# Kernel tuning notes

Hardware: AMD Instinct MI355X
Metric: run time of the kernel (lower is better)

Reference implementation:

```python
import jax, jax.numpy as jnp
import numpy as np

B, S, D, H = 2, 4096, 512, 8
HD = D // H  # head_dim = 64


def setup_inputs() -> dict:
    key = jax.random.key(0)
    ks = jax.random.split(key, 12)
    scale = 0.02
    inp = {
        "q": jax.random.normal(ks[0], (B, S, D), dtype=jnp.float32),
        "k": jax.random.normal(ks[1], (B, S, D), dtype=jnp.float32),
        "v": jax.random.normal(ks[2], (B, S, D), dtype=jnp.float32),
        "mask": jax.random.randint(ks[3], (B, S, S), 0, 2, dtype=jnp.int32),
        "wq_kernel": jax.random.normal(ks[4], (D, D), dtype=jnp.float32) * scale,
        "wq_bias": jnp.zeros((D,), dtype=jnp.float32),
        "wk_kernel": jax.random.normal(ks[5], (D, D), dtype=jnp.float32) * scale,
        "wk_bias": jnp.zeros((D,), dtype=jnp.float32),
        "wv_kernel": jax.random.normal(ks[6], (D, D), dtype=jnp.float32) * scale,
        "wv_bias": jnp.zeros((D,), dtype=jnp.float32),
        "wo_kernel": jax.random.normal(ks[7], (D, D), dtype=jnp.float32) * scale,
        "wo_bias": jnp.zeros((D,), dtype=jnp.float32),
    }
    return inp


def reference(q, k, v, mask, wq_kernel, wq_bias, wk_kernel, wk_bias,
              wv_kernel, wv_bias, wo_kernel, wo_bias):
    # Dense projections
    qp = q @ wq_kernel + wq_bias            # [B,S,D]
    kp = k @ wk_kernel + wk_bias
    vp = v @ wv_kernel + wv_bias

    def split_heads(x):
        # [B,S,D] -> [B,H,S,HD]
        return x.reshape(B, S, H, HD).transpose(0, 2, 1, 3)

    qh, kh, vh = split_heads(qp), split_heads(kp), split_heads(vp)

    # Scaled dot-product attention (materializes full [B,H,S,S] scores,
    # faithful to the original unfused implementation's math)
    scores = jnp.einsum('bhqd,bhkd->bhqk', qh, kh) / jnp.sqrt(
        jnp.asarray(HD, dtype=jnp.float32))
    scores = scores + mask.astype(jnp.float32)[:, None, :, :] * (-1e9)
    attn = jax.nn.softmax(scores, axis=-1)
    out = jnp.einsum('bhqk,bhkd->bhqd', attn, vh)   # [B,H,S,HD]

    # merge heads: [B,H,S,HD] -> [B,S,D]
    out = out.transpose(0, 2, 1, 3).reshape(B, S, D)
    return out @ wo_kernel + wo_bias
```

## Files before the change

kernel.cpp:

```cpp
#include <hip/hip_runtime.h>
#include <stdint.h>

#define B_ 2
#define S_ 4096
#define D_ 512
#define H_ 8
#define HD_ 64
#define M_ (B_*S_)

typedef __attribute__((ext_vector_type(8))) short bf16x8;
typedef __attribute__((ext_vector_type(4))) float f32x4;

#define QSCALE (0.125f * 1.44269504088896341f)

__device__ __forceinline__ unsigned short f2bf(float f) {
  union { float f; unsigned u; } un; un.f = f;
  unsigned u = un.u;
  return (unsigned short)((u + 0x7fffu + ((u >> 16) & 1u)) >> 16);
}

__device__ __forceinline__ unsigned cvtpk(float lo, float hi) {
  unsigned r;
  asm("v_cvt_pk_bf16_f32 %0, %1, %2" : "=v"(r) : "v"(lo), "v"(hi));
  return r;
}

__device__ __forceinline__ void gl16(const void* g, void* l) {
  __builtin_amdgcn_global_load_lds(
      (const __attribute__((address_space(1))) void*)g,
      (__attribute__((address_space(3))) void*)l, 16, 0, 0);
}

__device__ __forceinline__ int kperm_inv(int p) {
  return ((p & 0x1C) << 1) | ((p & 0x20) >> 3) | (p & 3);
}

__global__ __launch_bounds__(256) void mpack(const int* __restrict__ mask,
                                             unsigned long long* __restrict__ bits) {
  const int nw = (gridDim.x * 256) >> 6;
  int w = (blockIdx.x * 256 + threadIdx.x) >> 6;
  int lane = threadIdx.x & 63;
  const int NWORD = (int)((size_t)B_ * S_ * S_ / 64);
  for (int word = w; word < NWORD; word += nw) {
    int m = mask[(size_t)word * 64 + lane];
    unsigned long long bal = __ballot(m != 0);
    if (lane == 0) bits[word] = bal;
  }
}

__global__ __launch_bounds__(256) void wtrans4(const float* __restrict__ w0, const float* __restrict__ w1,
                                               const float* __restrict__ w2, const float* __restrict__ w3,
                                               unsigned short* __restrict__ t0, unsigned short* __restrict__ t1,
                                               unsigned short* __restrict__ t2, unsigned short* __restrict__ t3) {
  const float* W = blockIdx.z==0?w0: blockIdx.z==1?w1: blockIdx.z==2?w2:w3;
  unsigned short* T = blockIdx.z==0?t0: blockIdx.z==1?t1: blockIdx.z==2?t2:t3;
  __shared__ float tile[32][33];
  int n0 = blockIdx.x*32, k0 = blockIdx.y*32;
  int tx = threadIdx.x & 31, ty = threadIdx.x >> 5;
  #pragma unroll
  for (int i=0;i<4;i++)
    tile[ty + i*8][tx] = W[(size_t)(k0 + ty + i*8)*D_ + n0 + tx];
  __syncthreads();
  #pragma unroll
  for (int i=0;i<4;i++)
    T[(size_t)(n0 + ty + i*8)*D_ + k0 + tx] = f2bf(tile[tx][ty + i*8]);
}

template<int OUT_MODE, int CONVA>
__device__ __forceinline__ void gemm_body(const void* __restrict__ Ap,
                                          const unsigned short* __restrict__ Wt,
                                          const float* __restrict__ bias,
                                          void* __restrict__ Out, float oscale) {
  __shared__ __align__(16) unsigned short lAB[2*128*64];
  unsigned short* lA = lAB;
  unsigned short* lB = lAB + 128*64;
  int bm = blockIdx.x, bn = blockIdx.y;
  int tid = threadIdx.x, lane = tid & 63, wid = tid >> 6;
  int g = lane >> 4, cc = lane & 15;
  int wm = wid >> 1, wn = wid & 1;

  f32x4 acc[4][4];
  #pragma unroll
  for (int mi=0;mi<4;mi++)
    #pragma unroll
    for (int ni=0;ni<4;ni++)
      acc[mi][ni] = (f32x4){0.f,0.f,0.f,0.f};

  for (int ks = 0; ks < D_; ks += 64) {
    __syncthreads();
    #pragma unroll
    for (int c4 = 0; c4 < 4; c4++) {
      int idx = wid*256 + c4*64 + lane;
      int row = idx >> 3, ch = idx & 7;
      int sw = ch ^ (row & 7);
      bf16x8 va;
      if (CONVA) {
        const float* a32 = (const float*)Ap + (size_t)(bm*128 + row)*D_ + ks + ch*8;
        float4 f0 = *(const float4*)a32;
        float4 f1 = *(const float4*)(a32 + 4);
        union { unsigned d[4]; bf16x8 v; } u;
        u.d[0] = cvtpk(f0.x, f0.y);
        u.d[1] = cvtpk(f0.z, f0.w);
        u.d[2] = cvtpk(f1.x, f1.y);
        u.d[3] = cvtpk(f1.z, f1.w);
        va = u.v;
      } else {
        va = *(const bf16x8*)((const unsigned short*)Ap + (size_t)(bm*128 + row)*D_ + ks + ch*8);
      }
      bf16x8 vb = *(const bf16x8*)(Wt + (size_t)(bn*128 + row)*D_ + ks + ch*8);
      *(bf16x8*)((char*)lA + row*128 + sw*16) = va;
      *(bf16x8*)((char*)lB + row*128 + sw*16) = vb;
    }
    __syncthreads();
    #pragma unroll
    for (int kk = 0; kk < 2; kk++) {
      bf16x8 af[4], bfv[4];
      #pragma unroll
      for (int mi=0;mi<4;mi++) {
        int row = wm*64 + mi*16 + cc;
        af[mi] = *(const bf16x8*)((const char*)lA + row*128 + (((4*kk+g) ^ (row&7))<<4));
      }
      #pragma unroll
      for (int ni=0;ni<4;ni++) {
        int row = wn*64 + ni*16 + cc;
        bfv[ni] = *(const bf16x8*)((const char*)lB + row*128 + (((4*kk+g) ^ (row&7))<<4));
      }
      #pragma unroll
      for (int mi=0;mi<4;mi++)
        #pragma unroll
        for (int ni=0;ni<4;ni++)
          acc[mi][ni] = __builtin_amdgcn_mfma_f32_16x16x32_bf16(af[mi], bfv[ni], acc[mi][ni], 0, 0, 0);
    }
  }

  if (OUT_MODE == 2) {
    __syncthreads();
    char* ldsT = (char*)lAB + wid*8192;
    #pragma unroll
    for (int ni=0;ni<4;ni++) {
      int n_l = ni*16 + cc;
      float bv = bias[bn*128 + wn*64 + n_l];
      #pragma unroll
      for (int mi=0;mi<4;mi++) {
        ushort4 pk;
        pk.x = f2bf(acc[mi][ni][0] + bv);
        pk.y = f2bf(acc[mi][ni][1] + bv);
        pk.z = f2bf(acc[mi][ni][2] + bv);
        pk.w = f2bf(acc[mi][ni][3] + bv);
        *(ushort4*)(ldsT + n_l*128 + ((32*mi + 8*g) ^ ((n_l&7)<<4))) = pk;
      }
    }
    asm volatile("s_waitcnt lgkmcnt(0)" ::: "memory");
    __builtin_amdgcn_sched_barrier(0);
    #pragma unroll
    for (int it=0; it<8; ++it) {
      int task = it*64 + lane;
      int row = task >> 3, ch = task & 7;
      bf16x8 vv = *(const bf16x8*)(ldsT + row*128 + ((ch ^ (row&7))<<4));
      int n_g = bn*128 + wn*64 + row;
      int m_g = bm*128 + wm*64 + ch*8;
      int bb = m_g >> 12, ss = m_g & (S_-1);
      int hh = n_g >> 6, hd = n_g & 63;
      *(bf16x8*)((unsigned short*)Out + (((size_t)(bb*H_+hh)*HD_ + hd)*S_ + ss)) = vv;
    }
    return;
  }

  #pragma unroll
  for (int ni=0;ni<4;ni++) {
    int n = bn*128 + wn*64 + ni*16 + cc;
    float bv = bias[n];
    #pragma unroll
    for (int mi=0;mi<4;mi++) {
      f32x4 vacc = acc[mi][ni];
      #pragma unroll
      for (int j=0;j<4;j++) {
        int r = bm*128 + wm*64 + mi*16 + 4*g + j;
        float val = (vacc[j] + bv) * oscale;
        if (OUT_MODE == 0) {
          int b = r >> 12, s = r & (S_-1);
          int h = n >> 6, hd = n & 63;
          ((unsigned short*)Out)[(((size_t)(b*H_ + h)*S_ + s) << 6) + hd] = f2bf(val);
        } else {
          ((float*)Out)[(size_t)r*D_ + n] = val;
        }
      }
    }
  }
}

__global__ __launch_bounds__(256,3) void qkv_gemm(
    const float* __restrict__ q32, const float* __restrict__ k32, const float* __restrict__ v32,
    const unsigned short* __restrict__ wqt, const unsigned short* __restrict__ wkt,
    const unsigned short* __restrict__ wvt,
    const float* __restrict__ bq, const float* __restrict__ bk, const float* __restrict__ bv,
    unsigned short* __restrict__ Qp, unsigned short* __restrict__ Kp,
    unsigned short* __restrict__ Vt) {
  if (blockIdx.z == 0)      gemm_body<0,1>(q32, wqt, bq, Qp, QSCALE);
  else if (blockIdx.z == 1) gemm_body<0,1>(k32, wkt, bk, Kp, 1.0f);
  else                      gemm_body<2,1>(v32, wvt, bv, Vt, 1.0f);
}

__global__ __launch_bounds__(256,3) void o_gemm(const unsigned short* __restrict__ att,
                                                const unsigned short* __restrict__ wot,
                                                const float* __restrict__ bo,
                                                float* __restrict__ out) {
  gemm_body<1,0>(att, wot, bo, out, 1.0f);
}


#define FA_ISSUE(NCUR, MN0, MN1)                                        \
    { char* kb = lds + (NCUR)*8192 + woff;                              \
      gl16(gkA, kb); gl16(gkB, kb + 4096);                              \
      gl16(gvA, kb + 16384); gl16(gvB, kb + 16384 + 4096);              \
      gkA += 64*HD_; gkB += 64*HD_; gvA += 64; gvB += 64;               \
      MN0 = *mb0p++; MN1 = *mb1p++; }

#define FA_TILE(CUR, MC0, MC1, DOISSUE, MN0, MN1)                             \
  { asm volatile("s_waitcnt vmcnt(0)" ::: "memory");                          \
    __builtin_amdgcn_s_barrier();                                             \
    if (DOISSUE) FA_ISSUE((CUR)^1, MN0, MN1)                                  \
    f32x4 st0[4], st1[4];                                                     \
    __builtin_amdgcn_s_setprio(1);                                            \
    _Pragma("unroll")                                                         \
    for (int t4=0;t4<4;t4++) {                                                \
      bf16x8 ak0 = *(const bf16x8*)(lds + (CUR)*8192 + rdO[t4][0]);           \
      bf16x8 ak1 = *(const bf16x8*)(lds + (CUR)*8192 + rdO[t4][1]);           \
      f32x4 s0 = (f32x4){0.f,0.f,0.f,0.f};                                    \
      s0 = __builtin_amdgcn_mfma_f32_16x16x32_bf16(ak0, aq00, s0, 0,0,0);     \
      s0 = __builtin_amdgcn_mfma_f32_16x16x32_bf16(ak1, aq01, s0, 0,0,0);     \
      f32x4 s1 = (f32x4){0.f,0.f,0.f,0.f};                                    \
      s1 = __builtin_amdgcn_mfma_f32_16x16x32_bf16(ak0, aq10, s1, 0,0,0);     \
      s1 = __builtin_amdgcn_mfma_f32_16x16x32_bf16(ak1, aq11, s1, 0,0,0);     \
      st0[t4] = s0; st1[t4] = s1;                                             \
    }                                                                         \
    __builtin_amdgcn_s_setprio(0);                                            \
    unsigned long long sh0 = MC0 >> g8, sh1 = MC1 >> g8;                      \
    unsigned lo0 = (unsigned)sh0, hi0 = (unsigned)(sh0 >> 32);                \
    unsigned lo1 = (unsigned)sh1, hi1 = (unsigned)(sh1 >> 32);                \
    union { unsigned d[2][4]; bf16x8 v[2]; } P0, P1;                          \
    _Pragma("unroll")                                                         \
    for (int t4=0;t4<4;t4++) {                                                \
      unsigned bm0 = (t4 & 1) ? hi0 : lo0;                                    \
      unsigned bm1 = (t4 & 1) ? hi1 : lo1;                                    \
      const int bb = (t4 >> 1) * 4;                                           \
      float a0 = __builtin_amdgcn_exp2f(st0[t4][0] - mj);                     \
      float a1 = __builtin_amdgcn_exp2f(st0[t4][1] - mj);                     \
      float a2 = __builtin_amdgcn_exp2f(st0[t4][2] - mj);                     \
      float a3 = __builtin_amdgcn_exp2f(st0[t4][3] - mj);                     \
      a0 = (bm0 & (1u<<(bb+0))) ? 0.f : a0;                                   \
      a1 = (bm0 & (1u<<(bb+1))) ? 0.f : a1;                                   \
      a2 = (bm0 & (1u<<(bb+2))) ? 0.f : a2;                                   \
      a3 = (bm0 & (1u<<(bb+3))) ? 0.f : a3;                                   \
      P0.d[t4&1][(t4>>1)*2]   = cvtpk(a0, a1);                                \
      P0.d[t4&1][(t4>>1)*2+1] = cvtpk(a2, a3);                                \
      float c0 = __builtin_amdgcn_exp2f(st1[t4][0] - mj);                     \
      float c1 = __builtin_amdgcn_exp2f(st1[t4][1] - mj);                     \
      float c2 = __builtin_amdgcn_exp2f(st1[t4][2] - mj);                     \
      float c3 = __builtin_amdgcn_exp2f(st1[t4][3] - mj);                     \
      c0 = (bm1 & (1u<<(bb+0))) ? 0.f : c0;                                   \
      c1 = (bm1 & (1u<<(bb+1))) ? 0.f : c1;                                   \
      c2 = (bm1 & (1u<<(bb+2))) ? 0.f : c2;                                   \
      c3 = (bm1 & (1u<<(bb+3))) ? 0.f : c3;                                   \
      P1.d[t4&1][(t4>>1)*2]   = cvtpk(c0, c1);                                \
      P1.d[t4&1][(t4>>1)*2+1] = cvtpk(c2, c3);                                \
    }                                                                         \
    __builtin_amdgcn_s_setprio(1);                                            \
    _Pragma("unroll")                                                         \
    for (int kk=0;kk<2;kk++) {                                                \
      lj40 = __builtin_amdgcn_mfma_f32_16x16x32_bf16(P0.v[kk], vones, lj40, 0,0,0); \
      lj41 = __builtin_amdgcn_mfma_f32_16x16x32_bf16(P1.v[kk], vones, lj41, 0,0,0); \
      _Pragma("unroll")                                                       \
      for (int t4=0;t4<4;t4++) {                                              \
        bf16x8 bv8 = *(const bf16x8*)(lds + 16384 + (CUR)*8192 + rdO[t4][kk]); \
        o20[t4] = __builtin_amdgcn_mfma_f32_16x16x32_bf16(P0.v[kk], bv8, o20[t4], 0,0,0); \
        o21[t4] = __builtin_amdgcn_mfma_f32_16x16x32_bf16(P1.v[kk], bv8, o21[t4], 0,0,0); \
      }                                                                       \
    }                                                                         \
    __builtin_amdgcn_s_setprio(0);                                            \
    float pm0 = fmaxf(fmaxf(fmaxf(st0[0][0],st0[0][1]),fmaxf(st0[0][2],st0[0][3])),  \
                fmaxf(fmaxf(fmaxf(st0[1][0],st0[1][1]),fmaxf(st0[1][2],st0[1][3])),  \
                fmaxf(fmaxf(fmaxf(st0[2][0],st0[2][1]),fmaxf(st0[2][2],st0[2][3])),  \
                      fmaxf(fmaxf(st0[3][0],st0[3][1]),fmaxf(st0[3][2],st0[3][3]))))); \
    float pm1 = fmaxf(fmaxf(fmaxf(st1[0][0],st1[0][1]),fmaxf(st1[0][2],st1[0][3])),  \
                fmaxf(fmaxf(fmaxf(st1[1][0],st1[1][1]),fmaxf(st1[1][2],st1[1][3])),  \
                fmaxf(fmaxf(fmaxf(st1[2][0],st1[2][1]),fmaxf(st1[2][2],st1[2][3])),  \
                      fmaxf(fmaxf(st1[3][0],st1[3][1]),fmaxf(st1[3][2],st1[3][3]))))); \
    float pm = fmaxf(pm0, pm1);                                               \
    if (__any(pm > mj + 7.f)) {                                               \
      pm = fmaxf(pm, __shfl_xor(pm, 16));                                     \
      pm = fmaxf(pm, __shfl_xor(pm, 32));                                     \
      float mn = fmaxf(mj, pm);                                               \
      float alpha = __builtin_amdgcn_exp2f(mj - mn);                          \
      mj = mn;                                                                \
      _Pragma("unroll")                                                       \
      for (int j=0;j<4;j++) {                                                 \
        float aj = __shfl(alpha, 4*g + j);                                    \
        lj40[j] *= aj; lj41[j] *= aj;                                         \
        _Pragma("unroll")                                                     \
        for (int t4=0;t4<4;t4++) { o20[t4][j] *= aj; o21[t4][j] *= aj; }      \
      }                                                                       \
    } }

__global__ __launch_bounds__(256,2) void fattn(const unsigned short* __restrict__ Qp,
                                               const unsigned short* __restrict__ Kp,
                                               const unsigned short* __restrict__ Vt,
                                               const unsigned long long* __restrict__ bits,
                                               unsigned short* __restrict__ attO) {
  __shared__ __align__(16) char lds[32768];
  const int tid = threadIdx.x, lane = tid & 63, wid = tid >> 6;
  const int g = lane >> 4, cc = lane & 15;
  const int g8 = g << 3;

  const int n = blockIdx.x;
  const int xcd = n & 7, idx = n >> 3;
  const int bh = xcd*2 + (idx >> 5);
  const int qb = idx & 31;
  const int b = bh >> 3;
  const int q0w = qb*128 + wid*32;

  const unsigned short* Qb = Qp + (size_t)bh*S_*HD_;
  const unsigned short* Kb = Kp + (size_t)bh*S_*HD_;
  const unsigned short* Vb = Vt + (size_t)bh*HD_*S_;

  bf16x8 aq00 = *(const bf16x8*)(Qb + (size_t)(q0w+cc)*HD_ + g8);
  bf16x8 aq01 = *(const bf16x8*)(Qb + (size_t)(q0w+cc)*HD_ + 32 + g8);
  bf16x8 aq10 = *(const bf16x8*)(Qb + (size_t)(q0w+16+cc)*HD_ + g8);
  bf16x8 aq11 = *(const bf16x8*)(Qb + (size_t)(q0w+16+cc)*HD_ + 32 + g8);

  int rdO[4][2];
  #pragma unroll
  for (int t4=0;t4<4;t4++) {
    int row = t4*16 + cc;
    int base = row*128 + ((g ^ (row&7)) << 4);
    rdO[t4][0] = base;
    rdO[t4][1] = base ^ 64;
  }

  const int p0 = wid*8 + (lane >> 3);
  const int sl = lane & 7;
  const int cK = sl ^ (p0 & 7);
  const unsigned short* gkA = Kb + (size_t)kperm_inv(p0)      *HD_ + cK*8;
  const unsigned short* gkB = Kb + (size_t)kperm_inv(p0 + 32) *HD_ + cK*8;
  const unsigned short* gvA = Vb + (size_t)p0*S_ + cK*8;
  const unsigned short* gvB = gvA + (size_t)32*S_;
  const int woff = wid*1024;

  const unsigned long long* mb0p = bits + ((size_t)(b*S_ + q0w +      cc)) * (S_/64);
  const unsigned long long* mb1p = bits + ((size_t)(b*S_ + q0w + 16 + cc)) * (S_/64);

  union { unsigned d[4]; bf16x8 v; } onesu;
  onesu.d[0] = onesu.d[1] = onesu.d[2] = onesu.d[3] = 0x3F803F80u;
  const bf16x8 vones = onesu.v;

  f32x4 o20[4], o21[4];
  #pragma unroll
  for (int t4=0;t4<4;t4++) { o20[t4] = (f32x4){0.f,0.f,0.f,0.f}; o21[t4] = (f32x4){0.f,0.f,0.f,0.f}; }
  f32x4 lj40 = (f32x4){0.f,0.f,0.f,0.f};
  f32x4 lj41 = (f32x4){0.f,0.f,0.f,0.f};
  float mj = 0.f;

  unsigned long long mA0=0, mA1=0, mB0=0, mB1=0;

  const int NT = S_/64;

  FA_ISSUE(0, mA0, mA1)

  #pragma unroll 1
  for (int t2 = 0; t2 < NT; t2 += 2) {
    FA_TILE(0, mA0, mA1, true,         mB0, mB1)
    FA_TILE(1, mB0, mB1, (t2+2 < NT),  mA0, mA1)
  }

  const int h = bh & (H_-1);
  #pragma unroll
  for (int j=0;j<4;j++) {
    float i0 = __builtin_amdgcn_rcpf(lj40[j]);
    float i1 = __builtin_amdgcn_rcpf(lj41[j]);
    int qr0 = q0w + 4*g + j;
    int qr1 = q0w + 16 + 4*g + j;
    unsigned short* orow0 = attO + ((size_t)b*S_ + qr0)*D_ + h*HD_;
    unsigned short* orow1 = attO + ((size_t)b*S_ + qr1)*D_ + h*HD_;
    #pragma unroll
    for (int t4=0;t4<4;t4++) {
      orow0[t4*16 + cc] = f2bf(o20[t4][j] * i0);
      orow1[t4*16 + cc] = f2bf(o21[t4][j] * i1);
    }
  }
}

extern "C" void kernel_launch(void* const* d_in, const int* in_sizes, int n_in,
                              void* d_out, int out_size, void* d_ws, size_t ws_size,
                              hipStream_t stream) {
  const float* q    = (const float*)d_in[0];
  const float* k    = (const float*)d_in[1];
  const float* v    = (const float*)d_in[2];
  const int*   mask = (const int*)  d_in[3];
  const float* wq   = (const float*)d_in[4];
  const float* bq   = (const float*)d_in[5];
  const float* wk   = (const float*)d_in[6];
  const float* bk   = (const float*)d_in[7];
  const float* wv   = (const float*)d_in[8];
  const float* bv   = (const float*)d_in[9];
  const float* wo   = (const float*)d_in[10];
  const float* bo   = (const float*)d_in[11];

  char* ws = (char*)d_ws;
  const size_t SZ_MAT = (size_t)M_ * D_ * 2;
  const size_t SZ_W   = (size_t)D_ * D_ * 2;
  unsigned short* wqt = (unsigned short*)(ws);
  unsigned short* wkt = (unsigned short*)(ws + SZ_W);
  unsigned short* wvt = (unsigned short*)(ws + 2*SZ_W);
  unsigned short* wot = (unsigned short*)(ws + 3*SZ_W);
  unsigned short* Qp  = (unsigned short*)(ws + 4*SZ_W);
  unsigned short* Kp  = (unsigned short*)(ws + 4*SZ_W + SZ_MAT);
  unsigned short* Vt  = (unsigned short*)(ws + 4*SZ_W + 2*SZ_MAT);
  unsigned short* att = (unsigned short*)(ws + 4*SZ_W + 3*SZ_MAT);
  unsigned long long* bits = (unsigned long long*)(ws + 4*SZ_W + 4*SZ_MAT);

  mpack<<<2048, 256, 0, stream>>>(mask, bits);
  wtrans4<<<dim3(16,16,4), 256, 0, stream>>>(wq, wk, wv, wo, wqt, wkt, wvt, wot);
  qkv_gemm<<<dim3(64,4,3), 256, 0, stream>>>(q, k, v, wqt, wkt, wvt,
                                             bq, bk, bv, Qp, Kp, Vt);
  fattn<<<512, 256, 0, stream>>>(Qp, Kp, Vt, bits, att);
  o_gemm<<<dim3(64,4), 256, 0, stream>>>(att, wot, bo, (float*)d_out);
}
```

Measured before the change: 202.6 us.

## Software-pipeline flash attention with 4-slot K/V ring and QK/softmax overlap

Restructures the attention loop into a 4-stage ring buffer in LDS, doubled to 64KB, with loads issued two tiles ahead and waits relaxed to vmcnt(6). The QK^T of tile t+1 is interleaved with the softmax and PV of tile t, so MFMA work can overlap the exp and masking work and global-load latency. The cost is more LDS per block, which may lower occupancy below the two blocks per CU in launch bounds, and more registers for two score buffers. Out-of-range prefetches are clamped to the last tile, so some redundant loads are issued at the tail.

```diff
diff --git a/kernel.cpp b/kernel.cpp
--- a/kernel.cpp
+++ b/kernel.cpp
@@ -12,6 +12,7 @@
 typedef __attribute__((ext_vector_type(4))) float f32x4;
 
 #define QSCALE (0.125f * 1.44269504088896341f)
+#define MFMA16(A,B,C) __builtin_amdgcn_mfma_f32_16x16x32_bf16((A),(B),(C),0,0,0)
 
 __device__ __forceinline__ unsigned short f2bf(float f) {
   union { float f; unsigned u; } un; un.f = f;
@@ -129,7 +130,7 @@
       for (int mi=0;mi<4;mi++)
         #pragma unroll
         for (int ni=0;ni<4;ni++)
-          acc[mi][ni] = __builtin_amdgcn_mfma_f32_16x16x32_bf16(af[mi], bfv[ni], acc[mi][ni], 0, 0, 0);
+          acc[mi][ni] = MFMA16(af[mi], bfv[ni], acc[mi][ni]);
     }
   }
 
@@ -209,97 +210,97 @@
 }
 
 
-#define FA_ISSUE(NCUR, MN0, MN1)                                        \
-    { char* kb = lds + (NCUR)*8192 + woff;                              \
-      gl16(gkA, kb); gl16(gkB, kb + 4096);                              \
-      gl16(gvA, kb + 16384); gl16(gvB, kb + 16384 + 4096);              \
-      gkA += 64*HD_; gkB += 64*HD_; gvA += 64; gvB += 64;               \
-      MN0 = *mb0p++; MN1 = *mb1p++; }
-
-#define FA_TILE(CUR, MC0, MC1, DOISSUE, MN0, MN1)                             \
-  { asm volatile("s_waitcnt vmcnt(0)" ::: "memory");                          \
-    __builtin_amdgcn_s_barrier();                                             \
-    if (DOISSUE) FA_ISSUE((CUR)^1, MN0, MN1)                                  \
-    f32x4 st0[4], st1[4];                                                     \
-    __builtin_amdgcn_s_setprio(1);                                            \
-    _Pragma("unroll")                                                         \
-    for (int t4=0;t4<4;t4++) {                                                \
-      bf16x8 ak0 = *(const bf16x8*)(lds + (CUR)*8192 + rdO[t4][0]);           \
-      bf16x8 ak1 = *(const bf16x8*)(lds + (CUR)*8192 + rdO[t4][1]);           \
-      f32x4 s0 = (f32x4){0.f,0.f,0.f,0.f};                                    \
-      s0 = __builtin_amdgcn_mfma_f32_16x16x32_bf16(ak0, aq00, s0, 0,0,0);     \
-      s0 = __builtin_amdgcn_mfma_f32_16x16x32_bf16(ak1, aq01, s0, 0,0,0);     \
-      f32x4 s1 = (f32x4){0.f,0.f,0.f,0.f};                                    \
-      s1 = __builtin_amdgcn_mfma_f32_16x16x32_bf16(ak0, aq10, s1, 0,0,0);     \
-      s1 = __builtin_amdgcn_mfma_f32_16x16x32_bf16(ak1, aq11, s1, 0,0,0);     \
-      st0[t4] = s0; st1[t4] = s1;                                             \
-    }                                                                         \
-    __builtin_amdgcn_s_setprio(0);                                            \
-    unsigned long long sh0 = MC0 >> g8, sh1 = MC1 >> g8;                      \
-    unsigned lo0 = (unsigned)sh0, hi0 = (unsigned)(sh0 >> 32);                \
-    unsigned lo1 = (unsigned)sh1, hi1 = (unsigned)(sh1 >> 32);                \
-    union { unsigned d[2][4]; bf16x8 v[2]; } P0, P1;                          \
-    _Pragma("unroll")                                                         \
-    for (int t4=0;t4<4;t4++) {                                                \
-      unsigned bm0 = (t4 & 1) ? hi0 : lo0;                                    \
-      unsigned bm1 = (t4 & 1) ? hi1 : lo1;                                    \
-      const int bb = (t4 >> 1) * 4;                                           \
-      float a0 = __builtin_amdgcn_exp2f(st0[t4][0] - mj);                     \
-      float a1 = __builtin_amdgcn_exp2f(st0[t4][1] - mj);                     \
-      float a2 = __builtin_amdgcn_exp2f(st0[t4][2] - mj);                     \
-      float a3 = __builtin_amdgcn_exp2f(st0[t4][3] - mj);                     \
-      a0 = (bm0 & (1u<<(bb+0))) ? 0.f : a0;                                   \
-      a1 = (bm0 & (1u<<(bb+1))) ? 0.f : a1;                                   \
-      a2 = (bm0 & (1u<<(bb+2))) ? 0.f : a2;                                   \
-      a3 = (bm0 & (1u<<(bb+3))) ? 0.f : a3;                                   \
-      P0.d[t4&1][(t4>>1)*2]   = cvtpk(a0, a1);                                \
-      P0.d[t4&1][(t4>>1)*2+1] = cvtpk(a2, a3);                                \
-      float c0 = __builtin_amdgcn_exp2f(st1[t4][0] - mj);                     \
-      float c1 = __builtin_amdgcn_exp2f(st1[t4][1] - mj);                     \
-      float c2 = __builtin_amdgcn_exp2f(st1[t4][2] - mj);                     \
-      float c3 = __builtin_amdgcn_exp2f(st1[t4][3] - mj);                     \
-      c0 = (bm1 & (1u<<(bb+0))) ? 0.f : c0;                                   \
-      c1 = (bm1 & (1u<<(bb+1))) ? 0.f : c1;                                   \
-      c2 = (bm1 & (1u<<(bb+2))) ? 0.f : c2;                                   \
-      c3 = (bm1 & (1u<<(bb+3))) ? 0.f : c3;                                   \
-      P1.d[t4&1][(t4>>1)*2]   = cvtpk(c0, c1);                                \
-      P1.d[t4&1][(t4>>1)*2+1] = cvtpk(c2, c3);                                \
-    }                                                                         \
-    __builtin_amdgcn_s_setprio(1);                                            \
-    _Pragma("unroll")                                                         \
-    for (int kk=0;kk<2;kk++) {                                                \
-      lj40 = __builtin_amdgcn_mfma_f32_16x16x32_bf16(P0.v[kk], vones, lj40, 0,0,0); \
-      lj41 = __builtin_amdgcn_mfma_f32_16x16x32_bf16(P1.v[kk], vones, lj41, 0,0,0); \
-      _Pragma("unroll")                                                       \
-      for (int t4=0;t4<4;t4++) {                                              \
-        bf16x8 bv8 = *(const bf16x8*)(lds + 16384 + (CUR)*8192 + rdO[t4][kk]); \
-        o20[t4] = __builtin_amdgcn_mfma_f32_16x16x32_bf16(P0.v[kk], bv8, o20[t4], 0,0,0); \
-        o21[t4] = __builtin_amdgcn_mfma_f32_16x16x32_bf16(P1.v[kk], bv8, o21[t4], 0,0,0); \
-      }                                                                       \
-    }                                                                         \
-    __builtin_amdgcn_s_setprio(0);                                            \
-    float pm0 = fmaxf(fmaxf(fmaxf(st0[0][0],st0[0][1]),fmaxf(st0[0][2],st0[0][3])),  \
-                fmaxf(fmaxf(fmaxf(st0[1][0],st0[1][1]),fmaxf(st0[1][2],st0[1][3])),  \
-                fmaxf(fmaxf(fmaxf(st0[2][0],st0[2][1]),fmaxf(st0[2][2],st0[2][3])),  \
-                      fmaxf(fmaxf(st0[3][0],st0[3][1]),fmaxf(st0[3][2],st0[3][3]))))); \
-    float pm1 = fmaxf(fmaxf(fmaxf(st1[0][0],st1[0][1]),fmaxf(st1[0][2],st1[0][3])),  \
-                fmaxf(fmaxf(fmaxf(st1[1][0],st1[1][1]),fmaxf(st1[1][2],st1[1][3])),  \
-                fmaxf(fmaxf(fmaxf(st1[2][0],st1[2][1]),fmaxf(st1[2][2],st1[2][3])),  \
-                      fmaxf(fmaxf(st1[3][0],st1[3][1]),fmaxf(st1[3][2],st1[3][3]))))); \
-    float pm = fmaxf(pm0, pm1);                                               \
-    if (__any(pm > mj + 7.f)) {                                               \
-      pm = fmaxf(pm, __shfl_xor(pm, 16));                                     \
-      pm = fmaxf(pm, __shfl_xor(pm, 32));                                     \
-      float mn = fmaxf(mj, pm);                                               \
-      float alpha = __builtin_amdgcn_exp2f(mj - mn);                          \
-      mj = mn;                                                                \
-      _Pragma("unroll")                                                       \
-      for (int j=0;j<4;j++) {                                                 \
-        float aj = __shfl(alpha, 4*g + j);                                    \
-        lj40[j] *= aj; lj41[j] *= aj;                                         \
-        _Pragma("unroll")                                                     \
-        for (int t4=0;t4<4;t4++) { o20[t4][j] *= aj; o21[t4][j] *= aj; }      \
-      }                                                                       \
+#define WAITBAR { asm volatile("s_waitcnt vmcnt(6)" ::: "memory"); \
+                  __builtin_amdgcn_s_barrier(); }
+
+#define ISSUE(SLOT, TIDX) { \
+    int tn_ = (TIDX) < NT ? (TIDX) : NT-1; \
+    char* kb_ = lds + (SLOT)*8192 + woff; \
+    char* vb_ = lds + 32768 + (SLOT)*8192 + woff; \
+    gl16(gkA + (size_t)tn_*(64*HD_), kb_); \
+    gl16(gkB + (size_t)tn_*(64*HD_), kb_ + 4096); \
+    gl16(gvA + tn_*64, vb_); \
+    gl16(gvB + tn_*64, vb_ + 4096); \
+    msk0[SLOT] = mb0p[tn_]; \
+    msk1[SLOT] = mb1p[tn_]; }
+
+#define QK(SLOT, S0, S1) { \
+    __builtin_amdgcn_s_setprio(1); \
+    _Pragma("unroll") \
+    for (int t4=0;t4<4;t4++) { \
+      bf16x8 ak0 = *(const bf16x8*)(lds + (SLOT)*8192 + rdO[t4][0]); \
+      bf16x8 ak1 = *(const bf16x8*)(lds + (SLOT)*8192 + rdO[t4][1]); \
+      f32x4 s0 = (f32x4){0.f,0.f,0.f,0.f}; \
+      s0 = MFMA16(ak0, aq00, s0); \
+      s0 = MFMA16(ak1, aq01, s0); \
+      f32x4 s1 = (f32x4){0.f,0.f,0.f,0.f}; \
+      s1 = MFMA16(ak0, aq10, s1); \
+      s1 = MFMA16(ak1, aq11, s1); \
+      S0[t4] = s0; S1[t4] = s1; \
+    } \
+    __builtin_amdgcn_s_setprio(0); }
+
+#define SMPV(S0, S1, VSLOT, MSLOT) { \
+    unsigned long long sh0 = msk0[MSLOT] >> g8, sh1 = msk1[MSLOT] >> g8; \
+    unsigned lo0=(unsigned)sh0, hi0=(unsigned)(sh0>>32); \
+    unsigned lo1=(unsigned)sh1, hi1=(unsigned)(sh1>>32); \
+    union { unsigned d[2][4]; bf16x8 v[2]; } P0_, P1_; \
+    _Pragma("unroll") \
+    for (int t4=0;t4<4;t4++) { \
+      unsigned bm0=(t4&1)?hi0:lo0, bm1=(t4&1)?hi1:lo1; \
+      const int bb=(t4>>1)*4; \
+      float a0=__builtin_amdgcn_exp2f(S0[t4][0]-mj); \
+      float a1=__builtin_amdgcn_exp2f(S0[t4][1]-mj); \
+      float a2=__builtin_amdgcn_exp2f(S0[t4][2]-mj); \
+      float a3=__builtin_amdgcn_exp2f(S0[t4][3]-mj); \
+      a0=(bm0&(1u<<(bb+0)))?0.f:a0; a1=(bm0&(1u<<(bb+1)))?0.f:a1; \
+      a2=(bm0&(1u<<(bb+2)))?0.f:a2; a3=(bm0&(1u<<(bb+3)))?0.f:a3; \
+      P0_.d[t4&1][(t4>>1)*2]   = cvtpk(a0,a1); \
+      P0_.d[t4&1][(t4>>1)*2+1] = cvtpk(a2,a3); \
+      float c0=__builtin_amdgcn_exp2f(S1[t4][0]-mj); \
+      float c1=__builtin_amdgcn_exp2f(S1[t4][1]-mj); \
+      float c2=__builtin_amdgcn_exp2f(S1[t4][2]-mj); \
+      float c3=__builtin_amdgcn_exp2f(S1[t4][3]-mj); \
+      c0=(bm1&(1u<<(bb+0)))?0.f:c0; c1=(bm1&(1u<<(bb+1)))?0.f:c1; \
+      c2=(bm1&(1u<<(bb+2)))?0.f:c2; c3=(bm1&(1u<<(bb+3)))?0.f:c3; \
+      P1_.d[t4&1][(t4>>1)*2]   = cvtpk(c0,c1); \
+      P1_.d[t4&1][(t4>>1)*2+1] = cvtpk(c2,c3); \
+    } \
+    __builtin_amdgcn_s_setprio(1); \
+    _Pragma("unroll") \
+    for (int kk=0;kk<2;kk++) { \
+      lj40 = MFMA16(P0_.v[kk], vones, lj40); \
+      lj41 = MFMA16(P1_.v[kk], vones, lj41); \
+      _Pragma("unroll") \
+      for (int t4=0;t4<4;t4++) { \
+        bf16x8 bv8 = *(const bf16x8*)(lds + 32768 + (VSLOT)*8192 + rdO[t4][kk]); \
+        o20[t4] = MFMA16(P0_.v[kk], bv8, o20[t4]); \
+        o21[t4] = MFMA16(P1_.v[kk], bv8, o21[t4]); \
+      } \
+    } \
+    __builtin_amdgcn_s_setprio(0); \
+    float pm0 = fmaxf(fmaxf(fmaxf(S0[0][0],S0[0][1]),fmaxf(S0[0][2],S0[0][3])),  \
+                fmaxf(fmaxf(fmaxf(S0[1][0],S0[1][1]),fmaxf(S0[1][2],S0[1][3])),  \
+                fmaxf(fmaxf(fmaxf(S0[2][0],S0[2][1]),fmaxf(S0[2][2],S0[2][3])),  \
+                      fmaxf(fmaxf(S0[3][0],S0[3][1]),fmaxf(S0[3][2],S0[3][3]))))); \
+    float pm1 = fmaxf(fmaxf(fmaxf(S1[0][0],S1[0][1]),fmaxf(S1[0][2],S1[0][3])),  \
+                fmaxf(fmaxf(fmaxf(S1[1][0],S1[1][1]),fmaxf(S1[1][2],S1[1][3])),  \
+                fmaxf(fmaxf(fmaxf(S1[2][0],S1[2][1]),fmaxf(S1[2][2],S1[2][3])),  \
+                      fmaxf(fmaxf(S1[3][0],S1[3][1]),fmaxf(S1[3][2],S1[3][3]))))); \
+    float pm = fmaxf(pm0, pm1); \
+    if (__any(pm > mj + 7.f)) { \
+      pm = fmaxf(pm, __shfl_xor(pm, 16)); \
+      pm = fmaxf(pm, __shfl_xor(pm, 32)); \
+      float mn = fmaxf(mj, pm); \
+      float alpha = __builtin_amdgcn_exp2f(mj - mn); \
+      mj = mn; \
+      _Pragma("unroll") \
+      for (int j=0;j<4;j++) { \
+        float aj = __shfl(alpha, 4*g + j); \
+        lj40[j] *= aj; lj41[j] *= aj; \
+        _Pragma("unroll") \
+        for (int t4=0;t4<4;t4++) { o20[t4][j] *= aj; o21[t4][j] *= aj; } \
+      } \
     } }
 
 __global__ __launch_bounds__(256,2) void fattn(const unsigned short* __restrict__ Qp,
@@ -307,7 +308,7 @@
                                                const unsigned short* __restrict__ Vt,
                                                const unsigned long long* __restrict__ bits,
                                                unsigned short* __restrict__ attO) {
-  __shared__ __align__(16) char lds[32768];
+  __shared__ __align__(16) char lds[65536];
   const int tid = threadIdx.x, lane = tid & 63, wid = tid >> 6;
   const int g = lane >> 4, cc = lane & 15;
   const int g8 = g << 3;
@@ -360,17 +361,28 @@
   f32x4 lj41 = (f32x4){0.f,0.f,0.f,0.f};
   float mj = 0.f;
 
-  unsigned long long mA0=0, mA1=0, mB0=0, mB1=0;
+  unsigned long long msk0[4], msk1[4];
+  f32x4 stA0[4], stA1[4], stB0[4], stB1[4];
 
   const int NT = S_/64;
 
-  FA_ISSUE(0, mA0, mA1)
+  ISSUE(0, 0)
+  ISSUE(1, 1)
+
+  WAITBAR ISSUE(2, 2) QK(0, stA0, stA1)
+  WAITBAR ISSUE(3, 3) QK(1, stB0, stB1) SMPV(stA0, stA1, 0, 0)
+  WAITBAR ISSUE(0, 4) QK(2, stA0, stA1) SMPV(stB0, stB1, 1, 1)
+  WAITBAR ISSUE(1, 5) QK(3, stB0, stB1) SMPV(stA0, stA1, 2, 2)
 
   #pragma unroll 1
-  for (int t2 = 0; t2 < NT; t2 += 2) {
-    FA_TILE(0, mA0, mA1, true,         mB0, mB1)
-    FA_TILE(1, mB0, mB1, (t2+2 < NT),  mA0, mA1)
-  }
+  for (int t = 4; t < NT; t += 4) {
+    WAITBAR ISSUE(2, t+2) QK(0, stA0, stA1) SMPV(stB0, stB1, 3, 3)
+    WAITBAR ISSUE(3, t+3) QK(1, stB0, stB1) SMPV(stA0, stA1, 0, 0)
+    WAITBAR ISSUE(0, t+4) QK(2, stA0, stA1) SMPV(stB0, stB1, 1, 1)
+    WAITBAR ISSUE(1, t+5) QK(3, stB0, stB1) SMPV(stA0, stA1, 2, 2)
+  }
+
+  SMPV(stB0, stB1, 3, 3)
 
   const int h = bh & (H_-1);
   #pragma unroll
```

After: 189.3 us. -6.6%, faster.
